# Kernel optimization log

Hardware: AMD Instinct MI355X
Metric: run time of the kernel (lower is better)

Reference implementation:

```python
import jax, jax.numpy as jnp
import numpy as np

B, CIN, COUT, K, E, H, W = 32, 128, 256, 3, 8, 64, 64


def setup_inputs() -> dict:
    key = jax.random.key(0)
    k1, k2, k3, k4 = jax.random.split(key, 4)
    x = jax.random.normal(k1, (B, CIN, H, W), dtype=jnp.float32)
    expert_weight = jax.random.normal(k2, (E, COUT, CIN, K, K), dtype=jnp.float32)
    # nn.Linear(in_channels, num_experts): weight [E, CIN], bias [E]
    bound = 1.0 / np.sqrt(CIN)
    routing_w = jax.random.uniform(k3, (E, CIN), minval=-bound, maxval=bound, dtype=jnp.float32)
    routing_b = jax.random.uniform(k4, (E,), minval=-bound, maxval=bound, dtype=jnp.float32)
    return {"x": x, "expert_weight": expert_weight, "routing_w": routing_w, "routing_b": routing_b}


def reference(x, expert_weight, routing_w, routing_b):
    # routing: global-avg-pool -> linear -> softmax over experts
    pooled = x.mean(axis=(2, 3))                             # [B, CIN]
    logits = pooled @ routing_w.T + routing_b                # [B, E]
    rweights = jax.nn.softmax(logits, axis=-1)               # [B, E]
    # per-sample combined conv weights: [B, COUT, CIN, K, K]
    cw = jnp.einsum('be,eoikl->boikl', rweights, expert_weight)

    def conv_one(xi, wi):
        # xi: [CIN, H, W], wi: [COUT, CIN, K, K]; VALID conv, stride 1
        return jax.lax.conv_general_dilated(
            xi[None], wi, window_strides=(1, 1), padding='VALID',
            dimension_numbers=('NCHW', 'OIHW', 'NCHW'))[0]

    return jax.vmap(conv_one)(x, cw)                         # [B, COUT, H-K+1, W-K+1]
```

## Files before the change

kernel.cpp:

```cpp
#include <hip/hip_runtime.h>
#include <hip/hip_bf16.h>


#define CC_B    32
#define CC_CIN  128
#define CC_COUT 256
#define CC_NP   3844
#define CC_NT   18

typedef __attribute__((ext_vector_type(8))) short bf16x8;
typedef __attribute__((ext_vector_type(4))) float f32x4;

__global__ void cc_nhwc(const float* __restrict__ x, __hip_bfloat16* __restrict__ xn,
                        float* __restrict__ psum) {
    const int b = blockIdx.x >> 6, y = blockIdx.x & 63;
    __shared__ float lds[64 * 129];
    __shared__ float sred[256];
    const int t = threadIdx.x;
    const float* src = x + (size_t)b * CC_CIN * 4096 + y * 64;
#pragma unroll
    for (int i = 0; i < 32; ++i) {
        const int idx = i * 256 + t;
        const int cin = idx >> 6, xx = idx & 63;
        lds[xx * 129 + cin] = src[(size_t)cin * 4096 + xx];
    }
    __syncthreads();
    __hip_bfloat16* dst = xn + ((size_t)b * 4096 + y * 64) * CC_CIN;
#pragma unroll
    for (int j = 0; j < 4; ++j) {
        const int cidx = j * 256 + t;
        const int xx = cidx >> 4, c8 = (cidx & 15) * 8;
        union { __hip_bfloat16 h[8]; uint4 v; } u;
#pragma unroll
        for (int jj = 0; jj < 8; ++jj) u.h[jj] = __float2bfloat16(lds[xx * 129 + c8 + jj]);
        *reinterpret_cast<uint4*>(dst + (size_t)xx * CC_CIN + c8) = u.v;
    }
    const int cin = t & 127, xh = (t >> 7) * 32;
    float s = 0.f;
#pragma unroll
    for (int xx = 0; xx < 32; ++xx) s += lds[(xh + xx) * 129 + cin];
    sred[t] = s;
    __syncthreads();
    if (t < 128) psum[((size_t)b * 64 + y) * CC_CIN + t] = sred[t] + sred[t + 128];
}

__global__ void cc_reduce(const float* __restrict__ psum, float* __restrict__ pooled) {
    const int b = blockIdx.x, c = threadIdx.x;
    const float* p = psum + (size_t)b * 64 * CC_CIN + c;
    float s = 0.f;
#pragma unroll 8
    for (int y = 0; y < 64; ++y) s += p[(size_t)y * CC_CIN];
    pooled[b * CC_CIN + c] = s * (1.f / 4096.f);
}

__global__ void cc_routing(const float* __restrict__ pooled,
                           const float* __restrict__ rw_w,
                           const float* __restrict__ rw_b,
                           float* __restrict__ rweights) {
    const int t = threadIdx.x;
    const int b = t >> 3, e = t & 7;
    const float* p = pooled + b * CC_CIN;
    const float* w = rw_w + e * CC_CIN;
    float acc = rw_b[e];
#pragma unroll 8
    for (int i = 0; i < CC_CIN; ++i) acc += p[i] * w[i];
    float m = acc;
#pragma unroll
    for (int off = 1; off < 8; off <<= 1) m = fmaxf(m, __shfl_xor(m, off, 64));
    const float ex = __expf(acc - m);
    float sum = ex;
#pragma unroll
    for (int off = 1; off < 8; off <<= 1) sum += __shfl_xor(sum, off, 64);
    rweights[t] = ex / sum;
}

__global__ void cc_combine(const float* __restrict__ ew,
                           const float* __restrict__ rw,
                           __hip_bfloat16* __restrict__ cw) {
    const int t9 = blockIdx.x >> 8;
    const int cout = blockIdx.x & 255;
    const int cin = threadIdx.x;
    __shared__ float rws[256];
    rws[cin] = rw[cin];
    rws[cin + 128] = rw[cin + 128];
    __syncthreads();
    float wv[8];
    const size_t base = ((size_t)cout * CC_CIN + cin) * 9 + t9;
#pragma unroll
    for (int e = 0; e < 8; ++e) wv[e] = ew[base + (size_t)e * (CC_COUT * CC_CIN * 9)];
#pragma unroll 4
    for (int b = 0; b < CC_B; ++b) {
        float acc = 0.f;
#pragma unroll
        for (int e = 0; e < 8; ++e) acc += rws[b * 8 + e] * wv[e];
        cw[(((size_t)b * 9 + t9) * CC_COUT + cout) * CC_CIN + cin] = __float2bfloat16(acc);
    }
}

__device__ __forceinline__ void gload_lds16(const void* g, void* l) {
    __builtin_amdgcn_global_load_lds(
        (const __attribute__((address_space(1))) unsigned int*)g,
        (__attribute__((address_space(3))) unsigned int*)l, 16, 0, 0);
}

__global__ __launch_bounds__(512, 2) void cc_conv(
    const __hip_bfloat16* __restrict__ xn,
    const __hip_bfloat16* __restrict__ cw,
    float* __restrict__ out)
{
    __shared__ __align__(16) char smem[131072];
    const int n0 = blockIdx.x * 256;
    const int b  = blockIdx.y;
    const int tid = threadIdx.x;
    const int wid = tid >> 6, lane = tid & 63;
    const int waveM = wid >> 2, waveN = wid & 3;

    f32x4 acc[8][4];
#pragma unroll
    for (int i = 0; i < 8; ++i)
#pragma unroll
        for (int j = 0; j < 4; ++j) acc[i][j] = (f32x4){0.f, 0.f, 0.f, 0.f};

    const int gsw = (lane & 7) ^ (lane >> 3);
    int laOff[4], lbOff[4];
#pragma unroll
    for (int i = 0; i < 4; ++i) {
        const int row = wid * 32 + i * 8 + (lane >> 3);
        laOff[i] = row * CC_CIN + gsw * 8;
        int p = n0 + row; if (p > CC_NP - 1) p = CC_NP - 1;
        const int oy = p / 62, ox = p - oy * 62;
        lbOff[i] = (oy * 64 + ox) * CC_CIN + gsw * 8;
    }

    const __hip_bfloat16* cwb = cw + (size_t)b * 9 * CC_COUT * CC_CIN;
    const __hip_bfloat16* xnb = xn + (size_t)b * 4096 * CC_CIN;

    auto stageK = [&](int t) {
        const int t9 = t >> 1;
        const int ky = (t9 * 11) >> 5;
        const int kx = t9 - ky * 3;
        const int aoff = t9 * (CC_COUT * CC_CIN) + (t & 1) * 64;
        const int boff = (ky * 64 + kx) * CC_CIN + (t & 1) * 64;
        char* Ab = smem + (t & 1) * 32768 + wid * 4096;
        char* Bb = smem + 65536 + (t & 1) * 32768 + wid * 4096;
#pragma unroll
        for (int i = 0; i < 4; ++i)
            gload_lds16(cwb + aoff + laOff[i], Ab + i * 1024);
#pragma unroll
        for (int i = 0; i < 4; ++i)
            gload_lds16(xnb + boff + lbOff[i], Bb + i * 1024);
    };

    const int rl = lane & 15, q = lane >> 4;
    auto computeK = [&](int t) {
        const char* Ab = smem + (t & 1) * 32768;
        const char* Bb = smem + 65536 + (t & 1) * 32768;
#pragma unroll
        for (int kk = 0; kk < 2; ++kk) {
            bf16x8 af[8], bfr[4];
#pragma unroll
            for (int mf = 0; mf < 8; ++mf) {
                const int r = waveM * 128 + mf * 16 + rl;
                af[mf] = *(const bf16x8*)(Ab + r * 128 + (((kk * 4 + q) ^ (r & 7)) * 16));
            }
#pragma unroll
            for (int nf = 0; nf < 4; ++nf) {
                const int r = waveN * 64 + nf * 16 + rl;
                bfr[nf] = *(const bf16x8*)(Bb + r * 128 + (((kk * 4 + q) ^ (r & 7)) * 16));
            }
#pragma unroll
            for (int mf = 0; mf < 8; ++mf)
#pragma unroll
                for (int nf = 0; nf < 4; ++nf)
                    acc[mf][nf] = __builtin_amdgcn_mfma_f32_16x16x32_bf16(
                        af[mf], bfr[nf], acc[mf][nf], 0, 0, 0);
        }
    };

    stageK(0);
    stageK(1);

#pragma unroll 1
    for (int t = 0; t < CC_NT - 1; ++t) {
        asm volatile("s_waitcnt vmcnt(8)\n\ts_barrier" ::: "memory");
        computeK(t);
        asm volatile("s_waitcnt lgkmcnt(0)\n\ts_barrier" ::: "memory");
        if (t + 2 < CC_NT) stageK(t + 2);
    }
    asm volatile("s_waitcnt vmcnt(0)\n\ts_barrier" ::: "memory");
    computeK(CC_NT - 1);

    const int q4 = (lane >> 4) * 4;
#pragma unroll
    for (int mf = 0; mf < 8; ++mf) {
        const int crow = waveM * 128 + mf * 16 + q4;
#pragma unroll
        for (int nf = 0; nf < 4; ++nf) {
            const int p = n0 + waveN * 64 + nf * 16 + (lane & 15);
            if (p < CC_NP) {
                const size_t ob = ((size_t)b * CC_COUT + crow) * CC_NP + p;
#pragma unroll
                for (int j = 0; j < 4; ++j) out[ob + (size_t)j * CC_NP] = acc[mf][nf][j];
            }
        }
    }
}

extern "C" void kernel_launch(void* const* d_in, const int* in_sizes, int n_in,
                              void* d_out, int out_size, void* d_ws, size_t ws_size,
                              hipStream_t stream) {
    const float* x   = (const float*)d_in[0];
    const float* ew  = (const float*)d_in[1];
    const float* rww = (const float*)d_in[2];
    const float* rwb = (const float*)d_in[3];
    float* out = (float*)d_out;
    char* ws = (char*)d_ws;

    __hip_bfloat16* xnhwc = (__hip_bfloat16*)ws;
    __hip_bfloat16* cwcmb = (__hip_bfloat16*)(ws + 33554432);
    float* psum   = (float*)(ws + 52428800);
    float* pooled = (float*)(ws + 53477376);
    float* rwts   = (float*)(ws + 53493760);

    cc_nhwc<<<dim3(CC_B * 64), dim3(256), 0, stream>>>(x, xnhwc, psum);
    cc_reduce<<<dim3(CC_B), dim3(128), 0, stream>>>(psum, pooled);
    cc_routing<<<dim3(1), dim3(256), 0, stream>>>(pooled, rww, rwb, rwts);
    cc_combine<<<dim3(9 * CC_COUT), dim3(128), 0, stream>>>(ew, rwts, cwcmb);
    cc_conv<<<dim3(16, CC_B), dim3(512), 0, stream>>>(xnhwc, cwcmb, out);
}
```

Baseline: 132.6 us.

## Split conv K-step into four interleaved MFMA phases with staged loads and setprio

Result: no change. 134.5 us (+1.4%).

```diff
diff --git a/kernel.cpp b/kernel.cpp
--- a/kernel.cpp
+++ b/kernel.cpp
@@ -135,60 +135,124 @@
     const __hip_bfloat16* cwb = cw + (size_t)b * 9 * CC_COUT * CC_CIN;
     const __hip_bfloat16* xnb = xn + (size_t)b * 4096 * CC_CIN;
 
-    auto stageK = [&](int t) {
+    auto stageA = [&](int t) {
+        const int t9 = t >> 1;
+        const int aoff = t9 * (CC_COUT * CC_CIN) + (t & 1) * 64;
+        char* Ab = smem + (t & 1) * 32768 + wid * 4096;
+#pragma unroll
+        for (int i = 0; i < 4; ++i)
+            gload_lds16(cwb + aoff + laOff[i], Ab + i * 1024);
+    };
+    auto stageB = [&](int t) {
         const int t9 = t >> 1;
         const int ky = (t9 * 11) >> 5;
         const int kx = t9 - ky * 3;
-        const int aoff = t9 * (CC_COUT * CC_CIN) + (t & 1) * 64;
         const int boff = (ky * 64 + kx) * CC_CIN + (t & 1) * 64;
-        char* Ab = smem + (t & 1) * 32768 + wid * 4096;
         char* Bb = smem + 65536 + (t & 1) * 32768 + wid * 4096;
-#pragma unroll
-        for (int i = 0; i < 4; ++i)
-            gload_lds16(cwb + aoff + laOff[i], Ab + i * 1024);
 #pragma unroll
         for (int i = 0; i < 4; ++i)
             gload_lds16(xnb + boff + lbOff[i], Bb + i * 1024);
     };
 
-    const int rl = lane & 15, q = lane >> 4;
-    auto computeK = [&](int t) {
+    const int rl = lane & 15, q = lane >> 4, l7 = lane & 7;
+
+    stageA(0); stageB(0);
+    stageA(1); stageB(1);
+
+#pragma unroll 1
+    for (int t = 0; t < CC_NT; ++t) {
         const char* Ab = smem + (t & 1) * 32768;
         const char* Bb = smem + 65536 + (t & 1) * 32768;
-#pragma unroll
-        for (int kk = 0; kk < 2; ++kk) {
-            bf16x8 af[8], bfr[4];
-#pragma unroll
-            for (int mf = 0; mf < 8; ++mf) {
+
+        if (t < CC_NT - 1) asm volatile("s_waitcnt vmcnt(8)" ::: "memory");
+        else               asm volatile("s_waitcnt vmcnt(0)" ::: "memory");
+        asm volatile("s_barrier" ::: "memory");
+
+        bf16x8 af[8], bf0[4], bf1[4];
+
+#pragma unroll
+        for (int mf = 0; mf < 4; ++mf)
+#pragma unroll
+            for (int kk = 0; kk < 2; ++kk) {
                 const int r = waveM * 128 + mf * 16 + rl;
-                af[mf] = *(const bf16x8*)(Ab + r * 128 + (((kk * 4 + q) ^ (r & 7)) * 16));
-            }
-#pragma unroll
-            for (int nf = 0; nf < 4; ++nf) {
+                af[mf * 2 + kk] = *(const bf16x8*)(Ab + r * 128 + (((kk * 4 + q) ^ l7) * 16));
+            }
+#pragma unroll
+        for (int nf = 0; nf < 2; ++nf)
+#pragma unroll
+            for (int kk = 0; kk < 2; ++kk) {
                 const int r = waveN * 64 + nf * 16 + rl;
-                bfr[nf] = *(const bf16x8*)(Bb + r * 128 + (((kk * 4 + q) ^ (r & 7)) * 16));
-            }
-#pragma unroll
-            for (int mf = 0; mf < 8; ++mf)
-#pragma unroll
-                for (int nf = 0; nf < 4; ++nf)
+                bf0[nf * 2 + kk] = *(const bf16x8*)(Bb + r * 128 + (((kk * 4 + q) ^ l7) * 16));
+            }
+        asm volatile("s_barrier" ::: "memory");
+        asm volatile("s_waitcnt lgkmcnt(0)" ::: "memory");
+        __builtin_amdgcn_s_setprio(1);
+#pragma unroll
+        for (int mf = 0; mf < 4; ++mf)
+#pragma unroll
+            for (int nf = 0; nf < 2; ++nf)
+#pragma unroll
+                for (int kk = 0; kk < 2; ++kk)
                     acc[mf][nf] = __builtin_amdgcn_mfma_f32_16x16x32_bf16(
-                        af[mf], bfr[nf], acc[mf][nf], 0, 0, 0);
-        }
-    };
-
-    stageK(0);
-    stageK(1);
-
-#pragma unroll 1
-    for (int t = 0; t < CC_NT - 1; ++t) {
-        asm volatile("s_waitcnt vmcnt(8)\n\ts_barrier" ::: "memory");
-        computeK(t);
-        asm volatile("s_waitcnt lgkmcnt(0)\n\ts_barrier" ::: "memory");
-        if (t + 2 < CC_NT) stageK(t + 2);
-    }
-    asm volatile("s_waitcnt vmcnt(0)\n\ts_barrier" ::: "memory");
-    computeK(CC_NT - 1);
+                        af[mf * 2 + kk], bf0[nf * 2 + kk], acc[mf][nf], 0, 0, 0);
+        __builtin_amdgcn_s_setprio(0);
+        asm volatile("s_barrier" ::: "memory");
+
+#pragma unroll
+        for (int nf = 0; nf < 2; ++nf)
+#pragma unroll
+            for (int kk = 0; kk < 2; ++kk) {
+                const int r = waveN * 64 + (nf + 2) * 16 + rl;
+                bf1[nf * 2 + kk] = *(const bf16x8*)(Bb + r * 128 + (((kk * 4 + q) ^ l7) * 16));
+            }
+        asm volatile("s_barrier" ::: "memory");
+        asm volatile("s_waitcnt lgkmcnt(0)" ::: "memory");
+        __builtin_amdgcn_s_setprio(1);
+#pragma unroll
+        for (int mf = 0; mf < 4; ++mf)
+#pragma unroll
+            for (int nf = 0; nf < 2; ++nf)
+#pragma unroll
+                for (int kk = 0; kk < 2; ++kk)
+                    acc[mf][nf + 2] = __builtin_amdgcn_mfma_f32_16x16x32_bf16(
+                        af[mf * 2 + kk], bf1[nf * 2 + kk], acc[mf][nf + 2], 0, 0, 0);
+        __builtin_amdgcn_s_setprio(0);
+        asm volatile("s_barrier" ::: "memory");
+
+#pragma unroll
+        for (int mf = 0; mf < 4; ++mf)
+#pragma unroll
+            for (int kk = 0; kk < 2; ++kk) {
+                const int r = waveM * 128 + (mf + 4) * 16 + rl;
+                af[mf * 2 + kk] = *(const bf16x8*)(Ab + r * 128 + (((kk * 4 + q) ^ l7) * 16));
+            }
+        if (t + 2 < CC_NT) stageB(t + 2);
+        asm volatile("s_barrier" ::: "memory");
+        asm volatile("s_waitcnt lgkmcnt(0)" ::: "memory");
+        __builtin_amdgcn_s_setprio(1);
+#pragma unroll
+        for (int mf = 0; mf < 4; ++mf)
+#pragma unroll
+            for (int nf = 0; nf < 2; ++nf)
+#pragma unroll
+                for (int kk = 0; kk < 2; ++kk)
+                    acc[mf + 4][nf] = __builtin_amdgcn_mfma_f32_16x16x32_bf16(
+                        af[mf * 2 + kk], bf0[nf * 2 + kk], acc[mf + 4][nf], 0, 0, 0);
+        __builtin_amdgcn_s_setprio(0);
+        asm volatile("s_barrier" ::: "memory");
+
+        if (t + 2 < CC_NT) stageA(t + 2);
+        __builtin_amdgcn_s_setprio(1);
+#pragma unroll
+        for (int mf = 0; mf < 4; ++mf)
+#pragma unroll
+            for (int nf = 0; nf < 2; ++nf)
+#pragma unroll
+                for (int kk = 0; kk < 2; ++kk)
+                    acc[mf + 4][nf + 2] = __builtin_amdgcn_mfma_f32_16x16x32_bf16(
+                        af[mf * 2 + kk], bf1[nf * 2 + kk], acc[mf + 4][nf + 2], 0, 0, 0);
+        __builtin_amdgcn_s_setprio(0);
+    }
 
     const int q4 = (lane >> 4) * 4;
 #pragma unroll
```

## Shrink conv tiles to 128x128 with 256 threads and XCD-aware block mapping

Applied to the files above, without the earlier changes.

Result: faster. 127.2 us (-4.1%).

```diff
diff --git a/kernel.cpp b/kernel.cpp
--- a/kernel.cpp
+++ b/kernel.cpp
@@ -103,21 +103,26 @@
         (__attribute__((address_space(3))) unsigned int*)l, 16, 0, 0);
 }
 
-__global__ __launch_bounds__(512, 2) void cc_conv(
+__global__ __launch_bounds__(256, 2) void cc_conv(
     const __hip_bfloat16* __restrict__ xn,
     const __hip_bfloat16* __restrict__ cw,
     float* __restrict__ out)
 {
-    __shared__ __align__(16) char smem[131072];
-    const int n0 = blockIdx.x * 256;
-    const int b  = blockIdx.y;
+    __shared__ __align__(16) char smem[65536];
+    const int l   = blockIdx.x;
+    const int xcd = l & 7, li = l >> 3;
+    const int b   = 4 * xcd + li / 62;
+    const int r2  = li % 62;
+    const int m0  = (r2 & 1) * 128;
+    const int n0  = (r2 >> 1) * 128;
+
     const int tid = threadIdx.x;
     const int wid = tid >> 6, lane = tid & 63;
-    const int waveM = wid >> 2, waveN = wid & 3;
-
-    f32x4 acc[8][4];
-#pragma unroll
-    for (int i = 0; i < 8; ++i)
+    const int waveM = wid >> 1, waveN = wid & 1;
+
+    f32x4 acc[4][4];
+#pragma unroll
+    for (int i = 0; i < 4; ++i)
 #pragma unroll
         for (int j = 0; j < 4; ++j) acc[i][j] = (f32x4){0.f, 0.f, 0.f, 0.f};
 
@@ -126,7 +131,7 @@
 #pragma unroll
     for (int i = 0; i < 4; ++i) {
         const int row = wid * 32 + i * 8 + (lane >> 3);
-        laOff[i] = row * CC_CIN + gsw * 8;
+        laOff[i] = (m0 + row) * CC_CIN + gsw * 8;
         int p = n0 + row; if (p > CC_NP - 1) p = CC_NP - 1;
         const int oy = p / 62, ox = p - oy * 62;
         lbOff[i] = (oy * 64 + ox) * CC_CIN + gsw * 8;
@@ -141,8 +146,8 @@
         const int kx = t9 - ky * 3;
         const int aoff = t9 * (CC_COUT * CC_CIN) + (t & 1) * 64;
         const int boff = (ky * 64 + kx) * CC_CIN + (t & 1) * 64;
-        char* Ab = smem + (t & 1) * 32768 + wid * 4096;
-        char* Bb = smem + 65536 + (t & 1) * 32768 + wid * 4096;
+        char* Ab = smem + (t & 1) * 16384 + wid * 4096;
+        char* Bb = smem + 32768 + (t & 1) * 16384 + wid * 4096;
 #pragma unroll
         for (int i = 0; i < 4; ++i)
             gload_lds16(cwb + aoff + laOff[i], Ab + i * 1024);
@@ -152,48 +157,52 @@
     };
 
     const int rl = lane & 15, q = lane >> 4;
-    auto computeK = [&](int t) {
-        const char* Ab = smem + (t & 1) * 32768;
-        const char* Bb = smem + 65536 + (t & 1) * 32768;
-#pragma unroll
-        for (int kk = 0; kk < 2; ++kk) {
-            bf16x8 af[8], bfr[4];
-#pragma unroll
-            for (int mf = 0; mf < 8; ++mf) {
-                const int r = waveM * 128 + mf * 16 + rl;
-                af[mf] = *(const bf16x8*)(Ab + r * 128 + (((kk * 4 + q) ^ (r & 7)) * 16));
-            }
-#pragma unroll
-            for (int nf = 0; nf < 4; ++nf) {
-                const int r = waveN * 64 + nf * 16 + rl;
-                bfr[nf] = *(const bf16x8*)(Bb + r * 128 + (((kk * 4 + q) ^ (r & 7)) * 16));
-            }
-#pragma unroll
-            for (int mf = 0; mf < 8; ++mf)
-#pragma unroll
-                for (int nf = 0; nf < 4; ++nf)
-                    acc[mf][nf] = __builtin_amdgcn_mfma_f32_16x16x32_bf16(
-                        af[mf], bfr[nf], acc[mf][nf], 0, 0, 0);
-        }
-    };
 
     stageK(0);
     stageK(1);
 
 #pragma unroll 1
-    for (int t = 0; t < CC_NT - 1; ++t) {
-        asm volatile("s_waitcnt vmcnt(8)\n\ts_barrier" ::: "memory");
-        computeK(t);
-        asm volatile("s_waitcnt lgkmcnt(0)\n\ts_barrier" ::: "memory");
+    for (int t = 0; t < CC_NT; ++t) {
+        const char* Ab = smem + (t & 1) * 16384;
+        const char* Bb = smem + 32768 + (t & 1) * 16384;
+
+        if (t < CC_NT - 1) asm volatile("s_waitcnt vmcnt(8)" ::: "memory");
+        else               asm volatile("s_waitcnt vmcnt(0)" ::: "memory");
+        asm volatile("s_barrier" ::: "memory");
+
+        bf16x8 af[8], bf[8];
+#pragma unroll
+        for (int mf = 0; mf < 4; ++mf)
+#pragma unroll
+            for (int kk = 0; kk < 2; ++kk) {
+                const int r = waveM * 64 + mf * 16 + rl;
+                af[mf * 2 + kk] = *(const bf16x8*)(Ab + r * 128 + (((kk * 4 + q) ^ (r & 7)) * 16));
+            }
+#pragma unroll
+        for (int nf = 0; nf < 4; ++nf)
+#pragma unroll
+            for (int kk = 0; kk < 2; ++kk) {
+                const int r = waveN * 64 + nf * 16 + rl;
+                bf[nf * 2 + kk] = *(const bf16x8*)(Bb + r * 128 + (((kk * 4 + q) ^ (r & 7)) * 16));
+            }
+#pragma unroll
+        for (int mf = 0; mf < 4; ++mf)
+#pragma unroll
+            for (int nf = 0; nf < 4; ++nf)
+#pragma unroll
+                for (int kk = 0; kk < 2; ++kk)
+                    acc[mf][nf] = __builtin_amdgcn_mfma_f32_16x16x32_bf16(
+                        af[mf * 2 + kk], bf[nf * 2 + kk], acc[mf][nf], 0, 0, 0);
+
+        asm volatile("s_waitcnt lgkmcnt(0)" ::: "memory");
+        asm volatile("s_barrier" ::: "memory");
         if (t + 2 < CC_NT) stageK(t + 2);
     }
-    asm volatile("s_waitcnt vmcnt(0)\n\ts_barrier" ::: "memory");
-    computeK(CC_NT - 1);
 
     const int q4 = (lane >> 4) * 4;
 #pragma unroll
-    for (int mf = 0; mf < 8; ++mf) {
-        const int crow = waveM * 128 + mf * 16 + q4;
+    for (int mf = 0; mf < 4; ++mf) {
+        const int crow = m0 + waveM * 64 + mf * 16 + q4;
 #pragma unroll
         for (int nf = 0; nf < 4; ++nf) {
             const int p = n0 + waveN * 64 + nf * 16 + (lane & 15);
@@ -226,5 +235,5 @@
     cc_reduce<<<dim3(CC_B), dim3(128), 0, stream>>>(psum, pooled);
     cc_routing<<<dim3(1), dim3(256), 0, stream>>>(pooled, rww, rwb, rwts);
     cc_combine<<<dim3(9 * CC_COUT), dim3(128), 0, stream>>>(ew, rwts, cwcmb);
-    cc_conv<<<dim3(16, CC_B), dim3(512), 0, stream>>>(xnhwc, cwcmb, out);
-}
+    cc_conv<<<dim3(1984), dim3(256), 0, stream>>>(xnhwc, cwcmb, out);
+}
```
